# Kernel optimization log

Measured on AMD Instinct MI355X. Metric: run time of the kernel, lower is better.

Reference implementation:

```python
import jax, jax.numpy as jnp
import numpy as np


def setup_inputs() -> dict:
    key = jax.random.key(0)
    x = jax.random.normal(key, (16, 64, 256, 256), dtype=jnp.float32)
    return {"x": x}


def reference(x) -> jnp.ndarray:
    B, C, H, W = x.shape
    hw = H * W
    q = x.reshape(B, C, hw)          # proj_query: [B, C, HW]
    k = x.reshape(B, hw, C)          # proj_key: view (reshape), NOT transpose — faithful to source
    attn = jax.nn.softmax(jnp.einsum('bcn,bnd->bcd', q, k), axis=-1)  # [B, C, C]
    out = jnp.einsum('bcd,bdn->bcn', attn, q).reshape(B, C, H, W)
    return out + x
```

## Files before the change

kernel.cpp:

```cpp
#include <hip/hip_runtime.h>

#define B_   16
#define C_   64
#define HW_  65536
#define CHW_ (C_ * HW_)

typedef short bf16x8 __attribute__((ext_vector_type(8)));
typedef float f32x4v __attribute__((ext_vector_type(4)));

__device__ __forceinline__ unsigned short bfrne(float f) {
    unsigned int u = __float_as_uint(f);
    u += 0x7FFFu + ((u >> 16) & 1u);
    return (unsigned short)(u >> 16);
}
__device__ __forceinline__ float bfdec(unsigned short h) {
    return __uint_as_float((unsigned int)h << 16);
}

__global__ __launch_bounds__(256, 2) void k1_gram(const float* __restrict__ x,
                                                  float* __restrict__ partial,
                                                  int nch, int nb) {
    const int ch  = blockIdx.x;
    const int b   = blockIdx.y;
    const int t   = threadIdx.x;
    const int w   = t >> 6;
    const int l   = t & 63;
    const int g   = l >> 4;
    const int col = l & 15;

    const float* xb = x + (size_t)b * CHW_;
    const int nq  = nb >> 2;
    const int nw0 = ch * nb + w * nq;

    f32x4v acc[4][4];
    #pragma unroll
    for (int ct = 0; ct < 4; ct++)
        #pragma unroll
        for (int dt = 0; dt < 4; dt++) acc[ct][dt] = (f32x4v)(0.f);

    for (int ns = nw0; ns < nw0 + nq; ns += 32) {
        bf16x8 ahi[4], alo[4];
        #pragma unroll
        for (int ct = 0; ct < 4; ct++) {
            const float* ap = xb + (size_t)(16 * ct + col) * HW_ + ns + 8 * g;
            float av[8];
            *(float4*)&av[0] = *(const float4*)ap;
            *(float4*)&av[4] = *(const float4*)(ap + 4);
            #pragma unroll
            for (int j = 0; j < 8; j++) {
                const unsigned short h = bfrne(av[j]);
                ahi[ct][j] = (short)h;
                alo[ct][j] = (short)bfrne(av[j] - bfdec(h));
            }
        }
        bf16x8 bhi[4], blo[4];
        #pragma unroll
        for (int dt = 0; dt < 4; dt++) {
            const float* bp = xb + (size_t)(ns + 8 * g) * C_ + 16 * dt + col;
            float bv[8];
            #pragma unroll
            for (int j = 0; j < 8; j++) bv[j] = bp[j * C_];
            #pragma unroll
            for (int j = 0; j < 8; j++) {
                const unsigned short h = bfrne(bv[j]);
                bhi[dt][j] = (short)h;
                blo[dt][j] = (short)bfrne(bv[j] - bfdec(h));
            }
        }
        #pragma unroll
        for (int ct = 0; ct < 4; ct++)
            #pragma unroll
            for (int dt = 0; dt < 4; dt++) {
                acc[ct][dt] = __builtin_amdgcn_mfma_f32_16x16x32_bf16(
                    ahi[ct], bhi[dt], acc[ct][dt], 0, 0, 0);
                acc[ct][dt] = __builtin_amdgcn_mfma_f32_16x16x32_bf16(
                    ahi[ct], blo[dt], acc[ct][dt], 0, 0, 0);
                acc[ct][dt] = __builtin_amdgcn_mfma_f32_16x16x32_bf16(
                    alo[ct], bhi[dt], acc[ct][dt], 0, 0, 0);
            }
    }

    __shared__ float sred[4096];
    for (int wr = 0; wr < 4; wr++) {
        if (w == wr) {
            #pragma unroll
            for (int ct = 0; ct < 4; ct++)
                #pragma unroll
                for (int dt = 0; dt < 4; dt++)
                    #pragma unroll
                    for (int r = 0; r < 4; r++) {
                        const int idx = (16 * ct + 4 * g + r) * 64 + 16 * dt + col;
                        if (wr == 0) sred[idx] = acc[ct][dt][r];
                        else         sred[idx] += acc[ct][dt][r];
                    }
        }
        __syncthreads();
    }

    float* pb = partial + (size_t)(b * nch + ch) * 4096;
    for (int i = 4 * t; i < 4096; i += 1024)
        *(float4*)&pb[i] = *(const float4*)&sred[i];
}

__global__ __launch_bounds__(256) void k2_softmax(const float* __restrict__ partial,
                                                  unsigned short* __restrict__ mbf,
                                                  int nch) {
    const int c = blockIdx.x;
    const int b = blockIdx.y;
    const int t = threadIdx.x;
    const int w = t >> 6;
    const int d = t & 63;

    float s = 0.f;
    for (int ch = w; ch < nch; ch += 4)
        s += partial[(size_t)(b * nch + ch) * 4096 + c * 64 + d];

    __shared__ float red[256];
    red[t] = s;
    __syncthreads();
    if (w == 0) {
        s = red[d] + red[64 + d] + red[128 + d] + red[192 + d];
        float m = s;
        #pragma unroll
        for (int off = 32; off > 0; off >>= 1) m = fmaxf(m, __shfl_xor(m, off));
        const float e = expf(s - m);
        float sum = e;
        #pragma unroll
        for (int off = 32; off > 0; off >>= 1) sum += __shfl_xor(sum, off);
        mbf[(size_t)b * 4096 + c * 64 + d] = bfrne(e / sum + (c == d ? 1.f : 0.f));
    }
}

__global__ __launch_bounds__(256, 3) void k3_out(const float* __restrict__ x,
                                                 const unsigned short* __restrict__ mbf,
                                                 float* __restrict__ out) {
    const int nbk  = blockIdx.x;
    const int b    = blockIdx.y;
    const int t    = threadIdx.x;
    const int w    = t >> 6;
    const int l    = t & 63;
    const int g    = l >> 4;
    const int col  = l & 15;

    const int n0 = nbk * 256 + w * 64;
    const float* xb = x + (size_t)b * CHW_;

    bf16x8 afr[4][2];
    const unsigned short* mb = mbf + (size_t)b * 4096;
    #pragma unroll
    for (int ct = 0; ct < 4; ct++)
        #pragma unroll
        for (int ks = 0; ks < 2; ks++)
            afr[ct][ks] = *(const bf16x8*)(mb + (16 * ct + col) * 64 + 32 * ks + 8 * g);

    f32x4v acc[4][4];
    #pragma unroll
    for (int ct = 0; ct < 4; ct++)
        #pragma unroll
        for (int nt = 0; nt < 4; nt++)
            acc[ct][nt] = (f32x4v)(0.f);

    #pragma unroll
    for (int nt = 0; nt < 4; nt++) {
        const float* xpf = xb + n0 + 16 * nt + col;
        float xv[2][8];
        #pragma unroll
        for (int ks = 0; ks < 2; ks++)
            #pragma unroll
            for (int j = 0; j < 8; j++)
                xv[ks][j] = xpf[(size_t)(32 * ks + 8 * g + j) * HW_];

        bf16x8 bfr[2];
        #pragma unroll
        for (int ks = 0; ks < 2; ks++)
            #pragma unroll
            for (int j = 0; j < 8; j++)
                bfr[ks][j] = (short)bfrne(xv[ks][j]);

        #pragma unroll
        for (int ct = 0; ct < 4; ct++)
            #pragma unroll
            for (int ks = 0; ks < 2; ks++)
                acc[ct][nt] = __builtin_amdgcn_mfma_f32_16x16x32_bf16(
                    afr[ct][ks], bfr[ks], acc[ct][nt], 0, 0, 0);
    }

    float* ob = out + (size_t)b * CHW_;
    #pragma unroll
    for (int ct = 0; ct < 4; ct++)
        #pragma unroll
        for (int nt = 0; nt < 4; nt++)
            #pragma unroll
            for (int r = 0; r < 4; r++)
                ob[(size_t)(16 * ct + 4 * g + r) * HW_ + n0 + 16 * nt + col] =
                    acc[ct][nt][r];
}

extern "C" void kernel_launch(void* const* d_in, const int* in_sizes, int n_in,
                              void* d_out, int out_size, void* d_ws, size_t ws_size,
                              hipStream_t stream) {
    const float* x = (const float*)d_in[0];
    float* out = (float*)d_out;

    float* wsf          = (float*)d_ws;
    unsigned short* mbf = (unsigned short*)wsf;
    float* partial      = wsf + (size_t)B_ * 4096;

    int nch = 64;
    while (nch > 1) {
        size_t need = (size_t)B_ * 4096 * sizeof(float)
                    + (size_t)B_ * nch * 4096 * sizeof(float);
        if (need <= ws_size) break;
        nch >>= 1;
    }
    const int nb = HW_ / nch;

    k1_gram<<<dim3(nch, B_), 256, 0, stream>>>(x, partial, nch, nb);
    k2_softmax<<<dim3(C_, B_), 256, 0, stream>>>(partial, mbf, nch);
    k3_out<<<dim3(HW_ / 256, B_), 256, 0, stream>>>(x, mbf, out);
}
```

Baseline: 227.5 us.

## Split channel tiles across wave pairs and software-pipeline loads in output kernel

Both the Gram and output kernels now split the 64 output channels across pairs of waves, so each wave holds half the accumulators. The point is to cut register pressure and allow more resident waves (k1 launch bound raised to 3). k3 halves its per-block column span, doubling the grid, and double-buffers the strided x loads so the next tile's loads overlap the current tile's conversion and MFMAs. The trade-off is that each wave in k1 and k3 now re-reads the B-operand/x tile that its sibling wave also reads, roughly doubling those loads.

```diff
diff --git a/kernel.cpp b/kernel.cpp
--- a/kernel.cpp
+++ b/kernel.cpp
@@ -17,7 +17,7 @@
     return __uint_as_float((unsigned int)h << 16);
 }
 
-__global__ __launch_bounds__(256, 2) void k1_gram(const float* __restrict__ x,
+__global__ __launch_bounds__(256, 3) void k1_gram(const float* __restrict__ x,
                                                   float* __restrict__ partial,
                                                   int nch, int nb) {
     const int ch  = blockIdx.x;
@@ -27,22 +27,24 @@
     const int l   = t & 63;
     const int g   = l >> 4;
     const int col = l & 15;
+    const int ctg = w >> 1;
+    const int nh  = w & 1;
 
     const float* xb = x + (size_t)b * CHW_;
-    const int nq  = nb >> 2;
-    const int nw0 = ch * nb + w * nq;
-
-    f32x4v acc[4][4];
-    #pragma unroll
-    for (int ct = 0; ct < 4; ct++)
+    const int nq  = nb >> 1;
+    const int nw0 = ch * nb + nh * nq;
+
+    f32x4v acc[2][4];
+    #pragma unroll
+    for (int ct = 0; ct < 2; ct++)
         #pragma unroll
         for (int dt = 0; dt < 4; dt++) acc[ct][dt] = (f32x4v)(0.f);
 
     for (int ns = nw0; ns < nw0 + nq; ns += 32) {
-        bf16x8 ahi[4], alo[4];
-        #pragma unroll
-        for (int ct = 0; ct < 4; ct++) {
-            const float* ap = xb + (size_t)(16 * ct + col) * HW_ + ns + 8 * g;
+        bf16x8 ahi[2], alo[2];
+        #pragma unroll
+        for (int ct = 0; ct < 2; ct++) {
+            const float* ap = xb + (size_t)(32 * ctg + 16 * ct + col) * HW_ + ns + 8 * g;
             float av[8];
             *(float4*)&av[0] = *(const float4*)ap;
             *(float4*)&av[4] = *(const float4*)(ap + 4);
@@ -68,7 +70,7 @@
             }
         }
         #pragma unroll
-        for (int ct = 0; ct < 4; ct++)
+        for (int ct = 0; ct < 2; ct++)
             #pragma unroll
             for (int dt = 0; dt < 4; dt++) {
                 acc[ct][dt] = __builtin_amdgcn_mfma_f32_16x16x32_bf16(
@@ -81,15 +83,16 @@
     }
 
     __shared__ float sred[4096];
-    for (int wr = 0; wr < 4; wr++) {
-        if (w == wr) {
-            #pragma unroll
-            for (int ct = 0; ct < 4; ct++)
+    for (int wr = 0; wr < 2; wr++) {
+        if (nh == wr) {
+            #pragma unroll
+            for (int ct = 0; ct < 2; ct++)
                 #pragma unroll
                 for (int dt = 0; dt < 4; dt++)
                     #pragma unroll
                     for (int r = 0; r < 4; r++) {
-                        const int idx = (16 * ct + 4 * g + r) * 64 + 16 * dt + col;
+                        const int idx = (32 * ctg + 16 * ct + 4 * g + r) * 64
+                                        + 16 * dt + col;
                         if (wr == 0) sred[idx] = acc[ct][dt][r];
                         else         sred[idx] += acc[ct][dt][r];
                     }
@@ -141,58 +144,85 @@
     const int l    = t & 63;
     const int g    = l >> 4;
     const int col  = l & 15;
-
-    const int n0 = nbk * 256 + w * 64;
+    const int ctg  = w >> 1;
+    const int nw   = w & 1;
+
+    const int n0 = nbk * 128 + nw * 64;
     const float* xb = x + (size_t)b * CHW_;
 
-    bf16x8 afr[4][2];
+    bf16x8 afr[2][2];
     const unsigned short* mb = mbf + (size_t)b * 4096;
     #pragma unroll
-    for (int ct = 0; ct < 4; ct++)
+    for (int ct = 0; ct < 2; ct++)
         #pragma unroll
         for (int ks = 0; ks < 2; ks++)
-            afr[ct][ks] = *(const bf16x8*)(mb + (16 * ct + col) * 64 + 32 * ks + 8 * g);
-
-    f32x4v acc[4][4];
-    #pragma unroll
-    for (int ct = 0; ct < 4; ct++)
+            afr[ct][ks] = *(const bf16x8*)(mb + (32 * ctg + 16 * ct + col) * 64
+                                           + 32 * ks + 8 * g);
+
+    f32x4v acc[2][4];
+    #pragma unroll
+    for (int ct = 0; ct < 2; ct++)
         #pragma unroll
         for (int nt = 0; nt < 4; nt++)
             acc[ct][nt] = (f32x4v)(0.f);
 
-    #pragma unroll
-    for (int nt = 0; nt < 4; nt++) {
-        const float* xpf = xb + n0 + 16 * nt + col;
-        float xv[2][8];
-        #pragma unroll
-        for (int ks = 0; ks < 2; ks++)
-            #pragma unroll
-            for (int j = 0; j < 8; j++)
-                xv[ks][j] = xpf[(size_t)(32 * ks + 8 * g + j) * HW_];
-
-        bf16x8 bfr[2];
-        #pragma unroll
-        for (int ks = 0; ks < 2; ks++)
-            #pragma unroll
-            for (int j = 0; j < 8; j++)
-                bfr[ks][j] = (short)bfrne(xv[ks][j]);
-
-        #pragma unroll
-        for (int ct = 0; ct < 4; ct++)
-            #pragma unroll
-            for (int ks = 0; ks < 2; ks++)
-                acc[ct][nt] = __builtin_amdgcn_mfma_f32_16x16x32_bf16(
-                    afr[ct][ks], bfr[ks], acc[ct][nt], 0, 0, 0);
-    }
+#define K3_LOADF(P, nt)                                                    \
+    {                                                                      \
+        const float* xpf = xb + n0 + 16 * (nt) + col;                      \
+        _Pragma("unroll")                                                  \
+        for (int ks = 0; ks < 2; ks++)                                     \
+            _Pragma("unroll")                                              \
+            for (int j = 0; j < 8; j++)                                    \
+                P[8 * ks + j] = xpf[(size_t)(32 * ks + 8 * g + j) * HW_];  \
+    }
+
+#define K3_CONV(BF, P)                                                     \
+    _Pragma("unroll")                                                      \
+    for (int ks = 0; ks < 2; ks++)                                         \
+        _Pragma("unroll")                                                  \
+        for (int j = 0; j < 8; j++)                                        \
+            BF[ks][j] = (short)bfrne(P[8 * ks + j]);
+
+#define K3_MFMA(BF, nt)                                                    \
+    _Pragma("unroll")                                                      \
+    for (int ct = 0; ct < 2; ct++)                                         \
+        _Pragma("unroll")                                                  \
+        for (int ks = 0; ks < 2; ks++)                                     \
+            acc[ct][nt] = __builtin_amdgcn_mfma_f32_16x16x32_bf16(         \
+                afr[ct][ks], BF[ks], acc[ct][nt], 0, 0, 0);
+
+    float pA[16], pB[16];
+    bf16x8 bfA[2], bfB[2];
+
+    K3_LOADF(pA, 0);
+    K3_LOADF(pB, 1);
+
+    K3_CONV(bfA, pA);
+    K3_LOADF(pA, 2);
+    K3_MFMA(bfA, 0);
+
+    K3_CONV(bfB, pB);
+    K3_LOADF(pB, 3);
+    K3_MFMA(bfB, 1);
+
+    K3_CONV(bfA, pA);
+    K3_MFMA(bfA, 2);
+
+    K3_CONV(bfB, pB);
+    K3_MFMA(bfB, 3);
+
+#undef K3_LOADF
+#undef K3_CONV
+#undef K3_MFMA
 
     float* ob = out + (size_t)b * CHW_;
     #pragma unroll
-    for (int ct = 0; ct < 4; ct++)
+    for (int ct = 0; ct < 2; ct++)
         #pragma unroll
         for (int nt = 0; nt < 4; nt++)
             #pragma unroll
             for (int r = 0; r < 4; r++)
-                ob[(size_t)(16 * ct + 4 * g + r) * HW_ + n0 + 16 * nt + col] =
+                ob[(size_t)(32 * ctg + 16 * ct + 4 * g + r) * HW_ + n0 + 16 * nt + col] =
                     acc[ct][nt][r];
 }
 
@@ -217,5 +247,5 @@
 
     k1_gram<<<dim3(nch, B_), 256, 0, stream>>>(x, partial, nch, nb);
     k2_softmax<<<dim3(C_, B_), 256, 0, stream>>>(partial, mbf, nch);
-    k3_out<<<dim3(HW_ / 256, B_), 256, 0, stream>>>(x, mbf, out);
-}
+    k3_out<<<dim3(HW_ / 128, B_), 256, 0, stream>>>(x, mbf, out);
+}
```

Measured after the change: 255.7 us. 12.4% more time.
